# Kernel tuning notes

Measured on AMD Instinct MI355X. Metric: run time of the kernel, lower is better.

## Reference

```python
import jax, jax.numpy as jnp
import numpy as np

C = 256
NH = 8
G = 32  # groupnorm groups (min(32, C))
EPS = 1e-6


def setup_inputs() -> dict:
    key = jax.random.key(0)
    ks = jax.random.split(key, 7)
    B, D, H, W = 2, 16, 16, 16
    x = jax.random.normal(ks[0], (B, C, D, H, W), dtype=jnp.float32)
    gn_gamma = jnp.ones((C,), jnp.float32)
    gn_beta = jnp.zeros((C,), jnp.float32)
    s = 1.0 / np.sqrt(C)
    qkv_w = jax.random.normal(ks[1], (3 * C, C), jnp.float32) * s  # 1x1x1 conv weight
    qkv_b = jnp.zeros((3 * C,), jnp.float32)
    proj_w = jax.random.normal(ks[2], (C, C), jnp.float32) * s
    proj_b = jnp.zeros((C,), jnp.float32)
    return {"x": x, "gn_gamma": gn_gamma, "gn_beta": gn_beta,
            "qkv_w": qkv_w, "qkv_b": qkv_b, "proj_w": proj_w, "proj_b": proj_b}


def _group_norm(x, gamma, beta):
    # x: [B, C, S]
    B, Cc, S = x.shape
    xg = x.reshape(B, G, (Cc // G) * S)
    mu = xg.mean(axis=-1, keepdims=True)
    var = xg.var(axis=-1, keepdims=True)
    xg = (xg - mu) * jax.lax.rsqrt(var + EPS)
    x = xg.reshape(B, Cc, S)
    return x * gamma[None, :, None] + beta[None, :, None]


def reference(x, gn_gamma, gn_beta, qkv_w, qkv_b, proj_w, proj_b):
    B, Cc, D, H, W = x.shape
    S = D * H * W
    hd = Cc // NH
    xf = x.reshape(B, Cc, S)
    h = _group_norm(xf, gn_gamma, gn_beta)
    # 1x1x1 conv == channel matmul: [B, 3C, S]
    qkv = jnp.einsum('oc,bcs->bos', qkv_w, h) + qkv_b[None, :, None]
    # torch path: reshape(B,3C,S).permute(0,2,1).chunk -> q=channels[0:C]
    q, k, v = qkv[:, :Cc], qkv[:, Cc:2 * Cc], qkv[:, 2 * Cc:]
    # [B, C, S] -> [B, NH, S, hd]
    def to_heads(t):
        return t.reshape(B, NH, hd, S).transpose(0, 1, 3, 2)
    q, k, v = to_heads(q), to_heads(k), to_heads(v)
    scale = hd ** (-0.5)
    attn = jax.nn.softmax(jnp.einsum('bnqd,bnkd->bnqk', q, k) * scale, axis=-1)
    o = jnp.einsum('bnqk,bnkd->bnqd', attn, v)  # [B, NH, S, hd]
    o = o.transpose(0, 1, 3, 2).reshape(B, Cc, S)  # back to [B, C, S]
    o = jnp.einsum('oc,bcs->bos', proj_w, o) + proj_b[None, :, None]
    return x + o.reshape(B, Cc, D, H, W)
```

## Files before the change

### kernel.cpp

```cpp
#include <hip/hip_runtime.h>
#include <cstddef>

#define S_LEN 4096
#define C_DIM 256
#define NHEADS 8
#define HDIM 32

typedef __attribute__((ext_vector_type(8))) _Float16 half8;
typedef __attribute__((ext_vector_type(4))) _Float16 half4;
typedef __attribute__((ext_vector_type(2))) _Float16 h2t;
typedef __attribute__((ext_vector_type(2))) __fp16 fp16x2;
typedef __attribute__((ext_vector_type(4))) float floatx4;

#define SC2F ((float)(0.17677669529663687 * 1.4426950408889634))

__global__ __launch_bounds__(256) void prep_stats(
    const float* __restrict__ qkv_w, const float* __restrict__ proj_w,
    const float* __restrict__ qkv_b, const float* __restrict__ x,
    _Float16* __restrict__ wq, _Float16* __restrict__ wp,
    float* __restrict__ qbias, float* __restrict__ pstat)
{
  const int blk = blockIdx.x;
  const int tid = threadIdx.x;
  if (blk < 512) {
    __shared__ float red[2][4];
    const int gb = blk >> 3, e = blk & 7;
    const int g = gb & 31, b = gb >> 5;
    const float* xb = x + ((size_t)b * C_DIM + g * 8) * S_LEN + e * 4096;
    const float4* x4 = (const float4*)xb;
    float sum = 0.f, sumsq = 0.f;
    #pragma unroll
    for (int i = 0; i < 4; ++i) {
      float4 v = x4[tid + i * 256];
      sum += v.x + v.y + v.z + v.w;
      sumsq += v.x * v.x + v.y * v.y + v.z * v.z + v.w * v.w;
    }
    for (int off = 1; off < 64; off <<= 1) {
      sum += __shfl_xor(sum, off, 64);
      sumsq += __shfl_xor(sumsq, off, 64);
    }
    const int wv = tid >> 6, lane = tid & 63;
    if (lane == 0) { red[0][wv] = sum; red[1][wv] = sumsq; }
    __syncthreads();
    if (tid == 0) {
      pstat[(gb * 8 + e) * 2 + 0] = red[0][0] + red[0][1] + red[0][2] + red[0][3];
      pstat[(gb * 8 + e) * 2 + 1] = red[1][0] + red[1][1] + red[1][2] + red[1][3];
    }
  } else if (blk < 704) {
    const int i = (blk - 512) * 1024 + tid * 4;
    float4 v = *(const float4*)(qkv_w + i);
    const float sc = (i < 65536) ? SC2F : 1.f;
    half4 h = { (_Float16)(v.x * sc), (_Float16)(v.y * sc),
                (_Float16)(v.z * sc), (_Float16)(v.w * sc) };
    *(half4*)(wq + i) = h;
  } else if (blk < 768) {
    const int i = (blk - 704) * 1024 + tid * 4;
    float4 v = *(const float4*)(proj_w + i);
    half4 h = { (_Float16)v.x, (_Float16)v.y, (_Float16)v.z, (_Float16)v.w };
    *(half4*)(wp + i) = h;
  } else {
    #pragma unroll
    for (int j = 0; j < 3; ++j) {
      const int i = tid + j * 256;
      float bv = qkv_b[i];
      if (i < 256) bv *= SC2F;
      qbias[i] = bv;
    }
  }
}

__global__ __launch_bounds__(512) void qkv_gn_gemm(
    const _Float16* __restrict__ W, const float* __restrict__ bias,
    const float* __restrict__ x, const float* __restrict__ gamma,
    const float* __restrict__ beta, const float* __restrict__ pstat,
    _Float16* __restrict__ qo, _Float16* __restrict__ ko_,
    _Float16* __restrict__ vo)
{
  __shared__ __align__(16) _Float16 Ld[256 * 40];
  const int tid = threadIdx.x;
  const int b = blockIdx.y;
  const int s0 = blockIdx.x * 32;

  {
    const int c0 = (tid & 127) * 2, c1 = c0 + 1;
    const int sh = tid >> 7;
    const int gb = b * 32 + (c0 >> 3);
    float s = 0.f, sq = 0.f;
    #pragma unroll
    for (int e = 0; e < 8; ++e) {
      s  += pstat[(gb * 8 + e) * 2 + 0];
      sq += pstat[(gb * 8 + e) * 2 + 1];
    }
    const float mean = s * (1.f / 32768.f);
    const float rstd = rsqrtf(sq * (1.f / 32768.f) - mean * mean + 1e-6f);
    const float ga0 = gamma[c0] * rstd, be0 = beta[c0] - mean * ga0;
    const float ga1 = gamma[c1] * rstd, be1 = beta[c1] - mean * ga1;
    const float4* xa = (const float4*)(x + ((size_t)b * C_DIM + c0) * S_LEN + s0 + sh * 8);
    const float4* xc = (const float4*)(x + ((size_t)b * C_DIM + c1) * S_LEN + s0 + sh * 8);
    #pragma unroll
    for (int j = 0; j < 2; ++j) {
      float4 a = xa[j], c = xc[j];
      int sl = sh * 8 + j * 4;
      *(h2t*)&Ld[(sl + 0) * 264 + c0] = (h2t){ (_Float16)(a.x * ga0 + be0), (_Float16)(c.x * ga1 + be1) };
      *(h2t*)&Ld[(sl + 1) * 264 + c0] = (h2t){ (_Float16)(a.y * ga0 + be0), (_Float16)(c.y * ga1 + be1) };
      *(h2t*)&Ld[(sl + 2) * 264 + c0] = (h2t){ (_Float16)(a.z * ga0 + be0), (_Float16)(c.z * ga1 + be1) };
      *(h2t*)&Ld[(sl + 3) * 264 + c0] = (h2t){ (_Float16)(a.w * ga0 + be0), (_Float16)(c.w * ga1 + be1) };
    }
  }
  __syncthreads();

  const int lane = tid & 63, wv = tid >> 6;
  const int m = lane & 15, quad = lane >> 4;
  const _Float16* wrow[6];
  #pragma unroll
  for (int j = 0; j < 6; ++j)
    wrow[j] = W + (size_t)((wv + 8 * j) * 16 + m) * C_DIM + quad * 8;
  const _Float16* lp = &Ld[m * 264 + quad * 8];

  floatx4 acc[6][2];
  #pragma unroll
  for (int j = 0; j < 6; ++j) {
    acc[j][0] = (floatx4){0.f,0.f,0.f,0.f};
    acc[j][1] = (floatx4){0.f,0.f,0.f,0.f};
  }

  #pragma unroll 2
  for (int k0 = 0; k0 < C_DIM; k0 += 32) {
    half8 b0 = *(const half8*)(lp + k0);
    half8 b1 = *(const half8*)(lp + 16 * 264 + k0);
    #pragma unroll
    for (int j = 0; j < 6; ++j) {
      half8 a = *(const half8*)(wrow[j] + k0);
      acc[j][0] = __builtin_amdgcn_mfma_f32_16x16x32_f16(a, b0, acc[j][0], 0, 0, 0);
      acc[j][1] = __builtin_amdgcn_mfma_f32_16x16x32_f16(a, b1, acc[j][1], 0, 0, 0);
    }
  }

  __syncthreads();
  #pragma unroll
  for (int j = 0; j < 4; ++j) {
    const int ob = (wv + 8 * j) * 16 + quad * 4;
    const float bv0 = bias[ob], bv1 = bias[ob + 1],
                bv2 = bias[ob + 2], bv3 = bias[ob + 3];
    _Float16* dst = (ob < 256) ? qo : ko_;
    const int oo = ob & 255, n = oo >> 5, d0 = oo & 31;
    #pragma unroll
    for (int sub = 0; sub < 2; ++sub) {
      int s = s0 + sub * 16 + m;
      half4 h = { (_Float16)(acc[j][sub][0] + bv0), (_Float16)(acc[j][sub][1] + bv1),
                  (_Float16)(acc[j][sub][2] + bv2), (_Float16)(acc[j][sub][3] + bv3) };
      *(half4*)(dst + (((size_t)b * NHEADS + n) * S_LEN + s) * HDIM + d0) = h;
    }
  }
  _Float16* VLd = Ld;
  #pragma unroll
  for (int j = 4; j < 6; ++j) {
    const int ob = (wv + 8 * j) * 16 + quad * 4;
    const int lch = ob - 512;
    const float bv0 = bias[ob], bv1 = bias[ob + 1],
                bv2 = bias[ob + 2], bv3 = bias[ob + 3];
    #pragma unroll
    for (int sub = 0; sub < 2; ++sub) {
      int s = sub * 16 + m;
      VLd[(lch + 0) * 40 + s] = (_Float16)(acc[j][sub][0] + bv0);
      VLd[(lch + 1) * 40 + s] = (_Float16)(acc[j][sub][1] + bv1);
      VLd[(lch + 2) * 40 + s] = (_Float16)(acc[j][sub][2] + bv2);
      VLd[(lch + 3) * 40 + s] = (_Float16)(acc[j][sub][3] + bv3);
    }
  }
  __syncthreads();
  {
    const int ch = tid >> 1, sh = tid & 1;
    const int n = ch >> 5, d = ch & 31;
    _Float16* dst = vo + ((size_t)(b * NHEADS + n) * HDIM + d) * S_LEN + s0 + sh * 16;
    const _Float16* src = VLd + ch * 40 + sh * 16;
    *(half8*)(dst + 0) = *(const half8*)(src + 0);
    *(half8*)(dst + 8) = *(const half8*)(src + 8);
  }
}

__global__ __launch_bounds__(512) void attn_kernel(
    const _Float16* __restrict__ q, const _Float16* __restrict__ k,
    const _Float16* __restrict__ v, _Float16* __restrict__ o)
{
  __shared__ __align__(16) _Float16 Kl[2][128 * 40];
  __shared__ __align__(16) _Float16 Vl[2][32 * 136];
  const int tid = threadIdx.x;
  const int lane = tid & 63, wv = tid >> 6;
  const int m = lane & 15, quad = lane >> 4;
  const int n = blockIdx.y, b = blockIdx.z;
  const int qc = blockIdx.x;
  const int q0 = qc * 256 + wv * 32;
  const int bh = b * NHEADS + n;

  const _Float16* qb = q + (size_t)bh * S_LEN * HDIM;
  const _Float16* kb = k + (size_t)bh * S_LEN * HDIM;
  const _Float16* vb = v + (size_t)bh * HDIM * S_LEN;

  half8 qfA = *(const half8*)(qb + (size_t)(q0 + m) * HDIM + quad * 8);
  half8 qfB = *(const half8*)(qb + (size_t)(q0 + 16 + m) * HDIM + quad * 8);

  const int krow = wv * 16 + (lane >> 2), kc = (lane & 3) * 8;
  const int vrow = wv * 4 + (lane >> 4), vc = (lane & 15) * 8;
  const _Float16* kg = kb + (size_t)krow * HDIM + kc;
  const _Float16* vg = vb + (size_t)vrow * S_LEN + vc;
  const int klds = krow * 40 + kc;
  const int vlds = vrow * 136 + vc;

  int4 kreg = *(const int4*)kg;
  int4 vreg = *(const int4*)vg;
  const _Float16* kgp = kg + 128 * HDIM;
  const _Float16* vgp = vg + 128;

  floatx4 oA0 = {0.f,0.f,0.f,0.f}, oA1 = oA0, oB0 = oA0, oB1 = oA0;
  float lA0 = 0.f, lA1 = 0.f, lB0 = 0.f, lB1 = 0.f;
  const fp16x2 one2 = { (__fp16)1.0f, (__fp16)1.0f };
  const floatx4 zz = {0.f,0.f,0.f,0.f};

  #pragma unroll 2
  for (int it = 0; it < 32; ++it) {
    const int bufi = it & 1;
    *(int4*)(&Kl[bufi][klds]) = kreg;
    *(int4*)(&Vl[bufi][vlds]) = vreg;
    kreg = *(const int4*)kgp; kgp += 128 * HDIM;
    vreg = *(const int4*)vgp; vgp += 128;
    __syncthreads();
    const _Float16* Kb = Kl[bufi];
    const _Float16* Vb = Vl[bufi];

    #pragma unroll
    for (int t = 0; t < 8; ++t) {
      const int tt = (t + wv) & 7;
      half8 kf  = *(const half8*)(Kb + (tt * 16 + m) * 40 + quad * 8);
      half4 vf0 = *(const half4*)(Vb + m * 136 + tt * 16 + quad * 4);
      half4 vf1 = *(const half4*)(Vb + (16 + m) * 136 + tt * 16 + quad * 4);
      __builtin_amdgcn_s_setprio(1);
      floatx4 sA = __builtin_amdgcn_mfma_f32_16x16x32_f16(kf, qfA, zz, 0, 0, 0);
      floatx4 sB = __builtin_amdgcn_mfma_f32_16x16x32_f16(kf, qfB, zz, 0, 0, 0);
      __builtin_amdgcn_s_setprio(0);
      float eA0 = __builtin_amdgcn_exp2f(sA[0]);
      float eA1 = __builtin_amdgcn_exp2f(sA[1]);
      float eA2 = __builtin_amdgcn_exp2f(sA[2]);
      float eA3 = __builtin_amdgcn_exp2f(sA[3]);
      float eB0 = __builtin_amdgcn_exp2f(sB[0]);
      float eB1 = __builtin_amdgcn_exp2f(sB[1]);
      float eB2 = __builtin_amdgcn_exp2f(sB[2]);
      float eB3 = __builtin_amdgcn_exp2f(sB[3]);
      half4 pA, pB;
      fp16x2 pAlo = __builtin_amdgcn_cvt_pkrtz(eA0, eA1);
      fp16x2 pAhi = __builtin_amdgcn_cvt_pkrtz(eA2, eA3);
      fp16x2 pBlo = __builtin_amdgcn_cvt_pkrtz(eB0, eB1);
      fp16x2 pBhi = __builtin_amdgcn_cvt_pkrtz(eB2, eB3);
      *(fp16x2*)&pA = pAlo; *((fp16x2*)&pA + 1) = pAhi;
      *(fp16x2*)&pB = pBlo; *((fp16x2*)&pB + 1) = pBhi;
      lA0 = __builtin_amdgcn_fdot2(pAlo, one2, lA0, false);
      lA1 = __builtin_amdgcn_fdot2(pAhi, one2, lA1, false);
      lB0 = __builtin_amdgcn_fdot2(pBlo, one2, lB0, false);
      lB1 = __builtin_amdgcn_fdot2(pBhi, one2, lB1, false);
      __builtin_amdgcn_s_setprio(1);
      oA0 = __builtin_amdgcn_mfma_f32_16x16x16f16(vf0, pA, oA0, 0, 0, 0);
      oA1 = __builtin_amdgcn_mfma_f32_16x16x16f16(vf1, pA, oA1, 0, 0, 0);
      oB0 = __builtin_amdgcn_mfma_f32_16x16x16f16(vf0, pB, oB0, 0, 0, 0);
      oB1 = __builtin_amdgcn_mfma_f32_16x16x16f16(vf1, pB, oB1, 0, 0, 0);
      __builtin_amdgcn_s_setprio(0);
    }
  }
  float lA = lA0 + lA1, lB = lB0 + lB1;
  lA += __shfl_xor(lA, 16, 64); lA += __shfl_xor(lA, 32, 64);
  lB += __shfl_xor(lB, 16, 64); lB += __shfl_xor(lB, 32, 64);
  const float rA = 1.f / lA, rB = 1.f / lB;
  _Float16* obase = o + ((size_t)bh * S_LEN) * HDIM;
  {
    _Float16* oh = obase + (size_t)(q0 + m) * HDIM;
    half4 h0 = { (_Float16)(oA0[0] * rA), (_Float16)(oA0[1] * rA),
                 (_Float16)(oA0[2] * rA), (_Float16)(oA0[3] * rA) };
    half4 h1 = { (_Float16)(oA1[0] * rA), (_Float16)(oA1[1] * rA),
                 (_Float16)(oA1[2] * rA), (_Float16)(oA1[3] * rA) };
    *(half4*)(oh + quad * 4) = h0;
    *(half4*)(oh + 16 + quad * 4) = h1;
  }
  {
    _Float16* oh = obase + (size_t)(q0 + 16 + m) * HDIM;
    half4 h0 = { (_Float16)(oB0[0] * rB), (_Float16)(oB0[1] * rB),
                 (_Float16)(oB0[2] * rB), (_Float16)(oB0[3] * rB) };
    half4 h1 = { (_Float16)(oB1[0] * rB), (_Float16)(oB1[1] * rB),
                 (_Float16)(oB1[2] * rB), (_Float16)(oB1[3] * rB) };
    *(half4*)(oh + quad * 4) = h0;
    *(half4*)(oh + 16 + quad * 4) = h1;
  }
}

__global__ __launch_bounds__(256) void proj_gemm(
    const _Float16* __restrict__ W, const float* __restrict__ bias,
    const _Float16* __restrict__ o,
    const float* __restrict__ x, float* __restrict__ out)
{
  const int tid = threadIdx.x;
  const int lane = tid & 63, wv = tid >> 6;
  const int m = lane & 15, quad = lane >> 4;
  const int mtb = blockIdx.x * 8 + wv * 2;
  const int s0 = blockIdx.y * 64;
  const int b = blockIdx.z;

  const _Float16* wrow0 = W + (size_t)((mtb + 0) * 16 + m) * C_DIM + quad * 8;
  const _Float16* wrow1 = W + (size_t)((mtb + 1) * 16 + m) * C_DIM + quad * 8;
  floatx4 acc[2][4];
  #pragma unroll
  for (int j = 0; j < 2; ++j)
    #pragma unroll
    for (int s = 0; s < 4; ++s) acc[j][s] = (floatx4){0.f,0.f,0.f,0.f};

  #pragma unroll
  for (int k0 = 0; k0 < C_DIM; k0 += 32) {
    const int n = k0 >> 5;
    const int d0 = quad * 8;
    half8 bf[4];
    #pragma unroll
    for (int sub = 0; sub < 4; ++sub) {
      size_t idx = (((size_t)(b * NHEADS + n)) * S_LEN + s0 + sub * 16 + m) * HDIM + d0;
      bf[sub] = *(const half8*)(o + idx);
    }
    half8 af0 = *(const half8*)(wrow0 + k0);
    half8 af1 = *(const half8*)(wrow1 + k0);
    #pragma unroll
    for (int sub = 0; sub < 4; ++sub) {
      acc[0][sub] = __builtin_amdgcn_mfma_f32_16x16x32_f16(af0, bf[sub], acc[0][sub], 0, 0, 0);
      acc[1][sub] = __builtin_amdgcn_mfma_f32_16x16x32_f16(af1, bf[sub], acc[1][sub], 0, 0, 0);
    }
  }
  #pragma unroll
  for (int j = 0; j < 2; ++j)
    #pragma unroll
    for (int sub = 0; sub < 4; ++sub) {
      int s = s0 + sub * 16 + m;
      #pragma unroll
      for (int r = 0; r < 4; ++r) {
        int c = (mtb + j) * 16 + quad * 4 + r;
        size_t idx = ((size_t)b * C_DIM + c) * S_LEN + s;
        out[idx] = x[idx] + acc[j][sub][r] + bias[c];
      }
    }
}

extern "C" void kernel_launch(void* const* d_in, const int* in_sizes, int n_in,
                              void* d_out, int out_size, void* d_ws, size_t ws_size,
                              hipStream_t stream) {
  const float* x        = (const float*)d_in[0];
  const float* gn_gamma = (const float*)d_in[1];
  const float* gn_beta  = (const float*)d_in[2];
  const float* qkv_w    = (const float*)d_in[3];
  const float* qkv_b    = (const float*)d_in[4];
  const float* proj_w   = (const float*)d_in[5];
  const float* proj_b   = (const float*)d_in[6];
  float* out = (float*)d_out;

  const size_t n1 = (size_t)2 * S_LEN * C_DIM;
  char* ws = (char*)d_ws;
  _Float16* qx  = (_Float16*)ws;
  _Float16* kx  = qx + n1;
  _Float16* vx  = kx + n1;
  _Float16* wq  = vx + n1;
  _Float16* wp  = wq + 768 * 256;
  float*    qbias = (float*)(wp + 256 * 256);
  float*    pstat = qbias + 768;
  _Float16* ox  = (_Float16*)(pstat + 1024);

  prep_stats<<<769, 256, 0, stream>>>(qkv_w, proj_w, qkv_b, x, wq, wp, qbias, pstat);
  qkv_gn_gemm<<<dim3(128, 2), 512, 0, stream>>>(wq, qbias, x, gn_gamma, gn_beta, pstat, qx, kx, vx);
  attn_kernel<<<dim3(16, 8, 2), 512, 0, stream>>>(qx, kx, vx, ox);
  proj_gemm<<<dim3(2, 64, 2), 256, 0, stream>>>(wp, proj_b, ox, x, out);
}
```

Measured before the change: 144.6 us.

## Fuse all four stages into one cooperative persistent kernel with grid syncs

Merges the prep/stats, QKV GEMM with groupnorm, attention and projection kernels into one cooperative kernel of 256 blocks. Grid-wide syncs separate the stages, so the four separate launches and the gaps between them go away. The work is remapped per stage: stats jobs run two per block and the projection uses smaller tiles. In exchange, grid syncs and a fixed 256-block grid limit parallelism in stages that previously used more blocks, and one shared-memory allocation is reused across all stages.

```diff
diff --git a/kernel.cpp b/kernel.cpp
--- a/kernel.cpp
+++ b/kernel.cpp
@@ -1,5 +1,8 @@
 #include <hip/hip_runtime.h>
+#include <hip/hip_cooperative_groups.h>
 #include <cstddef>
+
+namespace cg = cooperative_groups;
 
 #define S_LEN 4096
 #define C_DIM 256
@@ -14,24 +17,54 @@
 
 #define SC2F ((float)(0.17677669529663687 * 1.4426950408889634))
 
-__global__ __launch_bounds__(256) void prep_stats(
-    const float* __restrict__ qkv_w, const float* __restrict__ proj_w,
-    const float* __restrict__ qkv_b, const float* __restrict__ x,
+__global__ __launch_bounds__(512) void fused_all(
+    const float* __restrict__ x, const float* __restrict__ gamma,
+    const float* __restrict__ beta, const float* __restrict__ qkv_w,
+    const float* __restrict__ qkv_b, const float* __restrict__ proj_w,
+    const float* __restrict__ proj_b, float* __restrict__ out,
     _Float16* __restrict__ wq, _Float16* __restrict__ wp,
-    float* __restrict__ qbias, float* __restrict__ pstat)
+    float* __restrict__ qbias, float* __restrict__ pstat,
+    _Float16* __restrict__ qx, _Float16* __restrict__ kx,
+    _Float16* __restrict__ vx, _Float16* __restrict__ ox)
 {
-  const int blk = blockIdx.x;
+  cg::grid_group grid = cg::this_grid();
+  __shared__ __align__(16) char smem[37888];
   const int tid = threadIdx.x;
-  if (blk < 512) {
-    __shared__ float red[2][4];
-    const int gb = blk >> 3, e = blk & 7;
+  const int bid = blockIdx.x;
+  const int lane = tid & 63, wv = tid >> 6;
+  const int m = lane & 15, quad = lane >> 4;
+
+  {
+    const int gi = bid * 512 + tid;
+    const int i = gi * 2;
+    if (i < 196608) {
+      float2 v = *(const float2*)(qkv_w + i);
+      const float sc = (i < 65536) ? SC2F : 1.f;
+      *(h2t*)(wq + i) = (h2t){ (_Float16)(v.x * sc), (_Float16)(v.y * sc) };
+    } else {
+      const int j = i - 196608;
+      float2 v = *(const float2*)(proj_w + j);
+      *(h2t*)(wp + j) = (h2t){ (_Float16)v.x, (_Float16)v.y };
+    }
+    if (bid == 0 && tid < 256) {
+      #pragma unroll
+      for (int j = 0; j < 3; ++j) {
+        const int i2 = tid + j * 256;
+        float bv = qkv_b[i2];
+        if (i2 < 256) bv *= SC2F;
+        qbias[i2] = bv;
+      }
+    }
+    float* red = (float*)smem;
+    const int h = tid >> 8, t = tid & 255;
+    const int job = bid * 2 + h;
+    const int gb = job >> 3, e = job & 7;
     const int g = gb & 31, b = gb >> 5;
-    const float* xb = x + ((size_t)b * C_DIM + g * 8) * S_LEN + e * 4096;
-    const float4* x4 = (const float4*)xb;
+    const float4* x4 = (const float4*)(x + ((size_t)b * C_DIM + g * 8) * S_LEN + e * 4096);
     float sum = 0.f, sumsq = 0.f;
     #pragma unroll
-    for (int i = 0; i < 4; ++i) {
-      float4 v = x4[tid + i * 256];
+    for (int i2 = 0; i2 < 4; ++i2) {
+      float4 v = x4[t + i2 * 256];
       sum += v.x + v.y + v.z + v.w;
       sumsq += v.x * v.x + v.y * v.y + v.z * v.z + v.w * v.w;
     }
@@ -39,307 +72,264 @@
       sum += __shfl_xor(sum, off, 64);
       sumsq += __shfl_xor(sumsq, off, 64);
     }
-    const int wv = tid >> 6, lane = tid & 63;
-    if (lane == 0) { red[0][wv] = sum; red[1][wv] = sumsq; }
+    const int w4 = (tid >> 6) & 3;
+    if (lane == 0) { red[(h * 2 + 0) * 4 + w4] = sum; red[(h * 2 + 1) * 4 + w4] = sumsq; }
     __syncthreads();
-    if (tid == 0) {
-      pstat[(gb * 8 + e) * 2 + 0] = red[0][0] + red[0][1] + red[0][2] + red[0][3];
-      pstat[(gb * 8 + e) * 2 + 1] = red[1][0] + red[1][1] + red[1][2] + red[1][3];
-    }
-  } else if (blk < 704) {
-    const int i = (blk - 512) * 1024 + tid * 4;
-    float4 v = *(const float4*)(qkv_w + i);
-    const float sc = (i < 65536) ? SC2F : 1.f;
-    half4 h = { (_Float16)(v.x * sc), (_Float16)(v.y * sc),
-                (_Float16)(v.z * sc), (_Float16)(v.w * sc) };
-    *(half4*)(wq + i) = h;
-  } else if (blk < 768) {
-    const int i = (blk - 704) * 1024 + tid * 4;
-    float4 v = *(const float4*)(proj_w + i);
-    half4 h = { (_Float16)v.x, (_Float16)v.y, (_Float16)v.z, (_Float16)v.w };
-    *(half4*)(wp + i) = h;
-  } else {
-    #pragma unroll
-    for (int j = 0; j < 3; ++j) {
-      const int i = tid + j * 256;
-      float bv = qkv_b[i];
-      if (i < 256) bv *= SC2F;
-      qbias[i] = bv;
+    if (t == 0) {
+      pstat[job * 2 + 0] = red[(h*2+0)*4+0] + red[(h*2+0)*4+1] + red[(h*2+0)*4+2] + red[(h*2+0)*4+3];
+      pstat[job * 2 + 1] = red[(h*2+1)*4+0] + red[(h*2+1)*4+1] + red[(h*2+1)*4+2] + red[(h*2+1)*4+3];
     }
   }
-}
-
-__global__ __launch_bounds__(512) void qkv_gn_gemm(
-    const _Float16* __restrict__ W, const float* __restrict__ bias,
-    const float* __restrict__ x, const float* __restrict__ gamma,
-    const float* __restrict__ beta, const float* __restrict__ pstat,
-    _Float16* __restrict__ qo, _Float16* __restrict__ ko_,
-    _Float16* __restrict__ vo)
-{
-  __shared__ __align__(16) _Float16 Ld[256 * 40];
-  const int tid = threadIdx.x;
-  const int b = blockIdx.y;
-  const int s0 = blockIdx.x * 32;
+  __threadfence();
+  grid.sync();
 
   {
-    const int c0 = (tid & 127) * 2, c1 = c0 + 1;
-    const int sh = tid >> 7;
-    const int gb = b * 32 + (c0 >> 3);
-    float s = 0.f, sq = 0.f;
-    #pragma unroll
-    for (int e = 0; e < 8; ++e) {
-      s  += pstat[(gb * 8 + e) * 2 + 0];
-      sq += pstat[(gb * 8 + e) * 2 + 1];
-    }
-    const float mean = s * (1.f / 32768.f);
-    const float rstd = rsqrtf(sq * (1.f / 32768.f) - mean * mean + 1e-6f);
-    const float ga0 = gamma[c0] * rstd, be0 = beta[c0] - mean * ga0;
-    const float ga1 = gamma[c1] * rstd, be1 = beta[c1] - mean * ga1;
-    const float4* xa = (const float4*)(x + ((size_t)b * C_DIM + c0) * S_LEN + s0 + sh * 8);
-    const float4* xc = (const float4*)(x + ((size_t)b * C_DIM + c1) * S_LEN + s0 + sh * 8);
-    #pragma unroll
-    for (int j = 0; j < 2; ++j) {
-      float4 a = xa[j], c = xc[j];
-      int sl = sh * 8 + j * 4;
-      *(h2t*)&Ld[(sl + 0) * 264 + c0] = (h2t){ (_Float16)(a.x * ga0 + be0), (_Float16)(c.x * ga1 + be1) };
-      *(h2t*)&Ld[(sl + 1) * 264 + c0] = (h2t){ (_Float16)(a.y * ga0 + be0), (_Float16)(c.y * ga1 + be1) };
-      *(h2t*)&Ld[(sl + 2) * 264 + c0] = (h2t){ (_Float16)(a.z * ga0 + be0), (_Float16)(c.z * ga1 + be1) };
-      *(h2t*)&Ld[(sl + 3) * 264 + c0] = (h2t){ (_Float16)(a.w * ga0 + be0), (_Float16)(c.w * ga1 + be1) };
+    _Float16* Ld = (_Float16*)smem;
+    const int b = bid >> 7;
+    const int s0 = (bid & 127) * 32;
+    {
+      const int c0 = (tid & 127) * 2, c1 = c0 + 1;
+      const int sh = tid >> 7;
+      const int gb = b * 32 + (c0 >> 3);
+      float s = 0.f, sq = 0.f;
+      #pragma unroll
+      for (int e = 0; e < 8; ++e) {
+        s  += pstat[(gb * 8 + e) * 2 + 0];
+        sq += pstat[(gb * 8 + e) * 2 + 1];
+      }
+      const float mean = s * (1.f / 32768.f);
+      const float rstd = rsqrtf(sq * (1.f / 32768.f) - mean * mean + 1e-6f);
+      const float ga0 = gamma[c0] * rstd, be0 = beta[c0] - mean * ga0;
+      const float ga1 = gamma[c1] * rstd, be1 = beta[c1] - mean * ga1;
+      const float4* xa = (const float4*)(x + ((size_t)b * C_DIM + c0) * S_LEN + s0 + sh * 8);
+      const float4* xc = (const float4*)(x + ((size_t)b * C_DIM + c1) * S_LEN + s0 + sh * 8);
+      #pragma unroll
+      for (int j = 0; j < 2; ++j) {
+        float4 a = xa[j], c = xc[j];
+        int sl = sh * 8 + j * 4;
+        *(h2t*)&Ld[(sl + 0) * 264 + c0] = (h2t){ (_Float16)(a.x * ga0 + be0), (_Float16)(c.x * ga1 + be1) };
+        *(h2t*)&Ld[(sl + 1) * 264 + c0] = (h2t){ (_Float16)(a.y * ga0 + be0), (_Float16)(c.y * ga1 + be1) };
+        *(h2t*)&Ld[(sl + 2) * 264 + c0] = (h2t){ (_Float16)(a.z * ga0 + be0), (_Float16)(c.z * ga1 + be1) };
+        *(h2t*)&Ld[(sl + 3) * 264 + c0] = (h2t){ (_Float16)(a.w * ga0 + be0), (_Float16)(c.w * ga1 + be1) };
+      }
+    }
+    __syncthreads();
+
+    const _Float16* wrow[6];
+    #pragma unroll
+    for (int j = 0; j < 6; ++j)
+      wrow[j] = wq + (size_t)((wv + 8 * j) * 16 + m) * C_DIM + quad * 8;
+    const _Float16* lp = &Ld[m * 264 + quad * 8];
+
+    floatx4 acc[6][2];
+    #pragma unroll
+    for (int j = 0; j < 6; ++j) {
+      acc[j][0] = (floatx4){0.f,0.f,0.f,0.f};
+      acc[j][1] = (floatx4){0.f,0.f,0.f,0.f};
+    }
+    #pragma unroll 2
+    for (int k0 = 0; k0 < C_DIM; k0 += 32) {
+      half8 b0 = *(const half8*)(lp + k0);
+      half8 b1 = *(const half8*)(lp + 16 * 264 + k0);
+      #pragma unroll
+      for (int j = 0; j < 6; ++j) {
+        half8 a = *(const half8*)(wrow[j] + k0);
+        acc[j][0] = __builtin_amdgcn_mfma_f32_16x16x32_f16(a, b0, acc[j][0], 0, 0, 0);
+        acc[j][1] = __builtin_amdgcn_mfma_f32_16x16x32_f16(a, b1, acc[j][1], 0, 0, 0);
+      }
+    }
+    __syncthreads();
+    #pragma unroll
+    for (int j = 0; j < 4; ++j) {
+      const int ob = (wv + 8 * j) * 16 + quad * 4;
+      const float bv0 = qbias[ob], bv1 = qbias[ob + 1],
+                  bv2 = qbias[ob + 2], bv3 = qbias[ob + 3];
+      _Float16* dst = (ob < 256) ? qx : kx;
+      const int oo = ob & 255, n = oo >> 5, d0 = oo & 31;
+      #pragma unroll
+      for (int sub = 0; sub < 2; ++sub) {
+        int s = s0 + sub * 16 + m;
+        half4 h = { (_Float16)(acc[j][sub][0] + bv0), (_Float16)(acc[j][sub][1] + bv1),
+                    (_Float16)(acc[j][sub][2] + bv2), (_Float16)(acc[j][sub][3] + bv3) };
+        *(half4*)(dst + (((size_t)b * NHEADS + n) * S_LEN + s) * HDIM + d0) = h;
+      }
+    }
+    _Float16* VLd = Ld;
+    #pragma unroll
+    for (int j = 4; j < 6; ++j) {
+      const int ob = (wv + 8 * j) * 16 + quad * 4;
+      const int lch = ob - 512;
+      const float bv0 = qbias[ob], bv1 = qbias[ob + 1],
+                  bv2 = qbias[ob + 2], bv3 = qbias[ob + 3];
+      #pragma unroll
+      for (int sub = 0; sub < 2; ++sub) {
+        int s = sub * 16 + m;
+        VLd[(lch + 0) * 40 + s] = (_Float16)(acc[j][sub][0] + bv0);
+        VLd[(lch + 1) * 40 + s] = (_Float16)(acc[j][sub][1] + bv1);
+        VLd[(lch + 2) * 40 + s] = (_Float16)(acc[j][sub][2] + bv2);
+        VLd[(lch + 3) * 40 + s] = (_Float16)(acc[j][sub][3] + bv3);
+      }
+    }
+    __syncthreads();
+    {
+      const int ch = tid >> 1, sh = tid & 1;
+      const int n = ch >> 5, d = ch & 31;
+      _Float16* dst = vx + ((size_t)(b * NHEADS + n) * HDIM + d) * S_LEN + s0 + sh * 16;
+      const _Float16* src = VLd + ch * 40 + sh * 16;
+      *(half8*)(dst + 0) = *(const half8*)(src + 0);
+      *(half8*)(dst + 8) = *(const half8*)(src + 8);
     }
   }
-  __syncthreads();
-
-  const int lane = tid & 63, wv = tid >> 6;
-  const int m = lane & 15, quad = lane >> 4;
-  const _Float16* wrow[6];
-  #pragma unroll
-  for (int j = 0; j < 6; ++j)
-    wrow[j] = W + (size_t)((wv + 8 * j) * 16 + m) * C_DIM + quad * 8;
-  const _Float16* lp = &Ld[m * 264 + quad * 8];
-
-  floatx4 acc[6][2];
-  #pragma unroll
-  for (int j = 0; j < 6; ++j) {
-    acc[j][0] = (floatx4){0.f,0.f,0.f,0.f};
-    acc[j][1] = (floatx4){0.f,0.f,0.f,0.f};
+  __threadfence();
+  grid.sync();
+
+  {
+    _Float16* KlB = (_Float16*)smem;
+    _Float16* VlB = (_Float16*)(smem + 20480);
+    const int qc = bid & 15, n = (bid >> 4) & 7, b = bid >> 7;
+    const int q0 = qc * 256 + wv * 32;
+    const int bh = b * NHEADS + n;
+
+    const _Float16* qb = qx + (size_t)bh * S_LEN * HDIM;
+    const _Float16* kb = kx + (size_t)bh * S_LEN * HDIM;
+    const _Float16* vb = vx + (size_t)bh * HDIM * S_LEN;
+
+    half8 qfA = *(const half8*)(qb + (size_t)(q0 + m) * HDIM + quad * 8);
+    half8 qfB = *(const half8*)(qb + (size_t)(q0 + 16 + m) * HDIM + quad * 8);
+
+    const int krow = wv * 16 + (lane >> 2), kc = (lane & 3) * 8;
+    const int vrow = wv * 4 + (lane >> 4), vc = (lane & 15) * 8;
+    const _Float16* kg = kb + (size_t)krow * HDIM + kc;
+    const _Float16* vg = vb + (size_t)vrow * S_LEN + vc;
+    const int klds = krow * 40 + kc;
+    const int vlds = vrow * 136 + vc;
+
+    int4 kreg = *(const int4*)kg;
+    int4 vreg = *(const int4*)vg;
+    const _Float16* kgp = kg + 128 * HDIM;
+    const _Float16* vgp = vg + 128;
+
+    floatx4 oA0 = {0.f,0.f,0.f,0.f}, oA1 = oA0, oB0 = oA0, oB1 = oA0;
+    float lA0 = 0.f, lA1 = 0.f, lB0 = 0.f, lB1 = 0.f;
+    const fp16x2 one2 = { (__fp16)1.0f, (__fp16)1.0f };
+    const floatx4 zz = {0.f,0.f,0.f,0.f};
+
+    #pragma unroll 2
+    for (int it = 0; it < 32; ++it) {
+      const int bufi = it & 1;
+      *(int4*)(KlB + bufi * 5120 + klds) = kreg;
+      *(int4*)(VlB + bufi * 4352 + vlds) = vreg;
+      kreg = *(const int4*)kgp; kgp += 128 * HDIM;
+      vreg = *(const int4*)vgp; vgp += 128;
+      __syncthreads();
+      const _Float16* Kb = KlB + bufi * 5120;
+      const _Float16* Vb = VlB + bufi * 4352;
+
+      #pragma unroll
+      for (int t = 0; t < 8; ++t) {
+        const int tt = (t + wv) & 7;
+        half8 kf  = *(const half8*)(Kb + (tt * 16 + m) * 40 + quad * 8);
+        half4 vf0 = *(const half4*)(Vb + m * 136 + tt * 16 + quad * 4);
+        half4 vf1 = *(const half4*)(Vb + (16 + m) * 136 + tt * 16 + quad * 4);
+        __builtin_amdgcn_s_setprio(1);
+        floatx4 sA = __builtin_amdgcn_mfma_f32_16x16x32_f16(kf, qfA, zz, 0, 0, 0);
+        floatx4 sB = __builtin_amdgcn_mfma_f32_16x16x32_f16(kf, qfB, zz, 0, 0, 0);
+        __builtin_amdgcn_s_setprio(0);
+        float eA0 = __builtin_amdgcn_exp2f(sA[0]);
+        float eA1 = __builtin_amdgcn_exp2f(sA[1]);
+        float eA2 = __builtin_amdgcn_exp2f(sA[2]);
+        float eA3 = __builtin_amdgcn_exp2f(sA[3]);
+        float eB0 = __builtin_amdgcn_exp2f(sB[0]);
+        float eB1 = __builtin_amdgcn_exp2f(sB[1]);
+        float eB2 = __builtin_amdgcn_exp2f(sB[2]);
+        float eB3 = __builtin_amdgcn_exp2f(sB[3]);
+        half4 pA, pB;
+        fp16x2 pAlo = __builtin_amdgcn_cvt_pkrtz(eA0, eA1);
+        fp16x2 pAhi = __builtin_amdgcn_cvt_pkrtz(eA2, eA3);
+        fp16x2 pBlo = __builtin_amdgcn_cvt_pkrtz(eB0, eB1);
+        fp16x2 pBhi = __builtin_amdgcn_cvt_pkrtz(eB2, eB3);
+        *(fp16x2*)&pA = pAlo; *((fp16x2*)&pA + 1) = pAhi;
+        *(fp16x2*)&pB = pBlo; *((fp16x2*)&pB + 1) = pBhi;
+        lA0 = __builtin_amdgcn_fdot2(pAlo, one2, lA0, false);
+        lA1 = __builtin_amdgcn_fdot2(pAhi, one2, lA1, false);
+        lB0 = __builtin_amdgcn_fdot2(pBlo, one2, lB0, false);
+        lB1 = __builtin_amdgcn_fdot2(pBhi, one2, lB1, false);
+        __builtin_amdgcn_s_setprio(1);
+        oA0 = __builtin_amdgcn_mfma_f32_16x16x16f16(vf0, pA, oA0, 0, 0, 0);
+        oA1 = __builtin_amdgcn_mfma_f32_16x16x16f16(vf1, pA, oA1, 0, 0, 0);
+        oB0 = __builtin_amdgcn_mfma_f32_16x16x16f16(vf0, pB, oB0, 0, 0, 0);
+        oB1 = __builtin_amdgcn_mfma_f32_16x16x16f16(vf1, pB, oB1, 0, 0, 0);
+        __builtin_amdgcn_s_setprio(0);
+      }
+    }
+    float lA = lA0 + lA1, lB = lB0 + lB1;
+    lA += __shfl_xor(lA, 16, 64); lA += __shfl_xor(lA, 32, 64);
+    lB += __shfl_xor(lB, 16, 64); lB += __shfl_xor(lB, 32, 64);
+    const float rA = 1.f / lA, rB = 1.f / lB;
+    _Float16* obase = ox + ((size_t)bh * S_LEN) * HDIM;
+    {
+      _Float16* oh = obase + (size_t)(q0 + m) * HDIM;
+      half4 h0 = { (_Float16)(oA0[0] * rA), (_Float16)(oA0[1] * rA),
+                   (_Float16)(oA0[2] * rA), (_Float16)(oA0[3] * rA) };
+      half4 h1 = { (_Float16)(oA1[0] * rA), (_Float16)(oA1[1] * rA),
+                   (_Float16)(oA1[2] * rA), (_Float16)(oA1[3] * rA) };
+      *(half4*)(oh + quad * 4) = h0;
+      *(half4*)(oh + 16 + quad * 4) = h1;
+    }
+    {
+      _Float16* oh = obase + (size_t)(q0 + 16 + m) * HDIM;
+      half4 h0 = { (_Float16)(oB0[0] * rB), (_Float16)(oB0[1] * rB),
+                   (_Float16)(oB0[2] * rB), (_Float16)(oB0[3] * rB) };
+      half4 h1 = { (_Float16)(oB1[0] * rB), (_Float16)(oB1[1] * rB),
+                   (_Float16)(oB1[2] * rB), (_Float16)(oB1[3] * rB) };
+      *(half4*)(oh + quad * 4) = h0;
+      *(half4*)(oh + 16 + quad * 4) = h1;
+    }
   }
-
-  #pragma unroll 2
-  for (int k0 = 0; k0 < C_DIM; k0 += 32) {
-    half8 b0 = *(const half8*)(lp + k0);
-    half8 b1 = *(const half8*)(lp + 16 * 264 + k0);
-    #pragma unroll
-    for (int j = 0; j < 6; ++j) {
-      half8 a = *(const half8*)(wrow[j] + k0);
-      acc[j][0] = __builtin_amdgcn_mfma_f32_16x16x32_f16(a, b0, acc[j][0], 0, 0, 0);
-      acc[j][1] = __builtin_amdgcn_mfma_f32_16x16x32_f16(a, b1, acc[j][1], 0, 0, 0);
-    }
+  __threadfence();
+  grid.sync();
+
+  {
+    const int b = bid >> 7;
+    const int s0 = (bid & 127) * 32;
+    const int mtb = wv * 2;
+    const _Float16* wrow0 = wp + (size_t)((mtb + 0) * 16 + m) * C_DIM + quad * 8;
+    const _Float16* wrow1 = wp + (size_t)((mtb + 1) * 16 + m) * C_DIM + quad * 8;
+    floatx4 acc[2][2];
+    acc[0][0] = (floatx4){0.f,0.f,0.f,0.f}; acc[0][1] = acc[0][0];
+    acc[1][0] = acc[0][0]; acc[1][1] = acc[0][0];
+
+    #pragma unroll
+    for (int k0 = 0; k0 < C_DIM; k0 += 32) {
+      const int n = k0 >> 5;
+      const int d0 = quad * 8;
+      half8 bf[2];
+      #pragma unroll
+      for (int sub = 0; sub < 2; ++sub) {
+        size_t idx = (((size_t)(b * NHEADS + n)) * S_LEN + s0 + sub * 16 + m) * HDIM + d0;
+        bf[sub] = *(const half8*)(ox + idx);
+      }
+      half8 af0 = *(const half8*)(wrow0 + k0);
+      half8 af1 = *(const half8*)(wrow1 + k0);
+      #pragma unroll
+      for (int sub = 0; sub < 2; ++sub) {
+        acc[0][sub] = __builtin_amdgcn_mfma_f32_16x16x32_f16(af0, bf[sub], acc[0][sub], 0, 0, 0);
+        acc[1][sub] = __builtin_amdgcn_mfma_f32_16x16x32_f16(af1, bf[sub], acc[1][sub], 0, 0, 0);
+      }
+    }
+    #pragma unroll
+    for (int j = 0; j < 2; ++j)
+      #pragma unroll
+      for (int sub = 0; sub < 2; ++sub) {
+        int s = s0 + sub * 16 + m;
+        #pragma unroll
+        for (int r = 0; r < 4; ++r) {
+          int c = (mtb + j) * 16 + quad * 4 + r;
+          size_t idx = ((size_t)b * C_DIM + c) * S_LEN + s;
+          out[idx] = x[idx] + acc[j][sub][r] + proj_b[c];
+        }
+      }
   }
-
-  __syncthreads();
-  #pragma unroll
-  for (int j = 0; j < 4; ++j) {
-    const int ob = (wv + 8 * j) * 16 + quad * 4;
-    const float bv0 = bias[ob], bv1 = bias[ob + 1],
-                bv2 = bias[ob + 2], bv3 = bias[ob + 3];
-    _Float16* dst = (ob < 256) ? qo : ko_;
-    const int oo = ob & 255, n = oo >> 5, d0 = oo & 31;
-    #pragma unroll
-    for (int sub = 0; sub < 2; ++sub) {
-      int s = s0 + sub * 16 + m;
-      half4 h = { (_Float16)(acc[j][sub][0] + bv0), (_Float16)(acc[j][sub][1] + bv1),
-                  (_Float16)(acc[j][sub][2] + bv2), (_Float16)(acc[j][sub][3] + bv3) };
-      *(half4*)(dst + (((size_t)b * NHEADS + n) * S_LEN + s) * HDIM + d0) = h;
-    }
-  }
-  _Float16* VLd = Ld;
-  #pragma unroll
-  for (int j = 4; j < 6; ++j) {
-    const int ob = (wv + 8 * j) * 16 + quad * 4;
-    const int lch = ob - 512;
-    const float bv0 = bias[ob], bv1 = bias[ob + 1],
-                bv2 = bias[ob + 2], bv3 = bias[ob + 3];
-    #pragma unroll
-    for (int sub = 0; sub < 2; ++sub) {
-      int s = sub * 16 + m;
-      VLd[(lch + 0) * 40 + s] = (_Float16)(acc[j][sub][0] + bv0);
-      VLd[(lch + 1) * 40 + s] = (_Float16)(acc[j][sub][1] + bv1);
-      VLd[(lch + 2) * 40 + s] = (_Float16)(acc[j][sub][2] + bv2);
-      VLd[(lch + 3) * 40 + s] = (_Float16)(acc[j][sub][3] + bv3);
-    }
-  }
-  __syncthreads();
-  {
-    const int ch = tid >> 1, sh = tid & 1;
-    const int n = ch >> 5, d = ch & 31;
-    _Float16* dst = vo + ((size_t)(b * NHEADS + n) * HDIM + d) * S_LEN + s0 + sh * 16;
-    const _Float16* src = VLd + ch * 40 + sh * 16;
-    *(half8*)(dst + 0) = *(const half8*)(src + 0);
-    *(half8*)(dst + 8) = *(const half8*)(src + 8);
-  }
-}
-
-__global__ __launch_bounds__(512) void attn_kernel(
-    const _Float16* __restrict__ q, const _Float16* __restrict__ k,
-    const _Float16* __restrict__ v, _Float16* __restrict__ o)
-{
-  __shared__ __align__(16) _Float16 Kl[2][128 * 40];
-  __shared__ __align__(16) _Float16 Vl[2][32 * 136];
-  const int tid = threadIdx.x;
-  const int lane = tid & 63, wv = tid >> 6;
-  const int m = lane & 15, quad = lane >> 4;
-  const int n = blockIdx.y, b = blockIdx.z;
-  const int qc = blockIdx.x;
-  const int q0 = qc * 256 + wv * 32;
-  const int bh = b * NHEADS + n;
-
-  const _Float16* qb = q + (size_t)bh * S_LEN * HDIM;
-  const _Float16* kb = k + (size_t)bh * S_LEN * HDIM;
-  const _Float16* vb = v + (size_t)bh * HDIM * S_LEN;
-
-  half8 qfA = *(const half8*)(qb + (size_t)(q0 + m) * HDIM + quad * 8);
-  half8 qfB = *(const half8*)(qb + (size_t)(q0 + 16 + m) * HDIM + quad * 8);
-
-  const int krow = wv * 16 + (lane >> 2), kc = (lane & 3) * 8;
-  const int vrow = wv * 4 + (lane >> 4), vc = (lane & 15) * 8;
-  const _Float16* kg = kb + (size_t)krow * HDIM + kc;
-  const _Float16* vg = vb + (size_t)vrow * S_LEN + vc;
-  const int klds = krow * 40 + kc;
-  const int vlds = vrow * 136 + vc;
-
-  int4 kreg = *(const int4*)kg;
-  int4 vreg = *(const int4*)vg;
-  const _Float16* kgp = kg + 128 * HDIM;
-  const _Float16* vgp = vg + 128;
-
-  floatx4 oA0 = {0.f,0.f,0.f,0.f}, oA1 = oA0, oB0 = oA0, oB1 = oA0;
-  float lA0 = 0.f, lA1 = 0.f, lB0 = 0.f, lB1 = 0.f;
-  const fp16x2 one2 = { (__fp16)1.0f, (__fp16)1.0f };
-  const floatx4 zz = {0.f,0.f,0.f,0.f};
-
-  #pragma unroll 2
-  for (int it = 0; it < 32; ++it) {
-    const int bufi = it & 1;
-    *(int4*)(&Kl[bufi][klds]) = kreg;
-    *(int4*)(&Vl[bufi][vlds]) = vreg;
-    kreg = *(const int4*)kgp; kgp += 128 * HDIM;
-    vreg = *(const int4*)vgp; vgp += 128;
-    __syncthreads();
-    const _Float16* Kb = Kl[bufi];
-    const _Float16* Vb = Vl[bufi];
-
-    #pragma unroll
-    for (int t = 0; t < 8; ++t) {
-      const int tt = (t + wv) & 7;
-      half8 kf  = *(const half8*)(Kb + (tt * 16 + m) * 40 + quad * 8);
-      half4 vf0 = *(const half4*)(Vb + m * 136 + tt * 16 + quad * 4);
-      half4 vf1 = *(const half4*)(Vb + (16 + m) * 136 + tt * 16 + quad * 4);
-      __builtin_amdgcn_s_setprio(1);
-      floatx4 sA = __builtin_amdgcn_mfma_f32_16x16x32_f16(kf, qfA, zz, 0, 0, 0);
-      floatx4 sB = __builtin_amdgcn_mfma_f32_16x16x32_f16(kf, qfB, zz, 0, 0, 0);
-      __builtin_amdgcn_s_setprio(0);
-      float eA0 = __builtin_amdgcn_exp2f(sA[0]);
-      float eA1 = __builtin_amdgcn_exp2f(sA[1]);
-      float eA2 = __builtin_amdgcn_exp2f(sA[2]);
-      float eA3 = __builtin_amdgcn_exp2f(sA[3]);
-      float eB0 = __builtin_amdgcn_exp2f(sB[0]);
-      float eB1 = __builtin_amdgcn_exp2f(sB[1]);
-      float eB2 = __builtin_amdgcn_exp2f(sB[2]);
-      float eB3 = __builtin_amdgcn_exp2f(sB[3]);
-      half4 pA, pB;
-      fp16x2 pAlo = __builtin_amdgcn_cvt_pkrtz(eA0, eA1);
-      fp16x2 pAhi = __builtin_amdgcn_cvt_pkrtz(eA2, eA3);
-      fp16x2 pBlo = __builtin_amdgcn_cvt_pkrtz(eB0, eB1);
-      fp16x2 pBhi = __builtin_amdgcn_cvt_pkrtz(eB2, eB3);
-      *(fp16x2*)&pA = pAlo; *((fp16x2*)&pA + 1) = pAhi;
-      *(fp16x2*)&pB = pBlo; *((fp16x2*)&pB + 1) = pBhi;
-      lA0 = __builtin_amdgcn_fdot2(pAlo, one2, lA0, false);
-      lA1 = __builtin_amdgcn_fdot2(pAhi, one2, lA1, false);
-      lB0 = __builtin_amdgcn_fdot2(pBlo, one2, lB0, false);
-      lB1 = __builtin_amdgcn_fdot2(pBhi, one2, lB1, false);
-      __builtin_amdgcn_s_setprio(1);
-      oA0 = __builtin_amdgcn_mfma_f32_16x16x16f16(vf0, pA, oA0, 0, 0, 0);
-      oA1 = __builtin_amdgcn_mfma_f32_16x16x16f16(vf1, pA, oA1, 0, 0, 0);
-      oB0 = __builtin_amdgcn_mfma_f32_16x16x16f16(vf0, pB, oB0, 0, 0, 0);
-      oB1 = __builtin_amdgcn_mfma_f32_16x16x16f16(vf1, pB, oB1, 0, 0, 0);
-      __builtin_amdgcn_s_setprio(0);
-    }
-  }
-  float lA = lA0 + lA1, lB = lB0 + lB1;
-  lA += __shfl_xor(lA, 16, 64); lA += __shfl_xor(lA, 32, 64);
-  lB += __shfl_xor(lB, 16, 64); lB += __shfl_xor(lB, 32, 64);
-  const float rA = 1.f / lA, rB = 1.f / lB;
-  _Float16* obase = o + ((size_t)bh * S_LEN) * HDIM;
-  {
-    _Float16* oh = obase + (size_t)(q0 + m) * HDIM;
-    half4 h0 = { (_Float16)(oA0[0] * rA), (_Float16)(oA0[1] * rA),
-                 (_Float16)(oA0[2] * rA), (_Float16)(oA0[3] * rA) };
-    half4 h1 = { (_Float16)(oA1[0] * rA), (_Float16)(oA1[1] * rA),
-                 (_Float16)(oA1[2] * rA), (_Float16)(oA1[3] * rA) };
-    *(half4*)(oh + quad * 4) = h0;
-    *(half4*)(oh + 16 + quad * 4) = h1;
-  }
-  {
-    _Float16* oh = obase + (size_t)(q0 + 16 + m) * HDIM;
-    half4 h0 = { (_Float16)(oB0[0] * rB), (_Float16)(oB0[1] * rB),
-                 (_Float16)(oB0[2] * rB), (_Float16)(oB0[3] * rB) };
-    half4 h1 = { (_Float16)(oB1[0] * rB), (_Float16)(oB1[1] * rB),
-                 (_Float16)(oB1[2] * rB), (_Float16)(oB1[3] * rB) };
-    *(half4*)(oh + quad * 4) = h0;
-    *(half4*)(oh + 16 + quad * 4) = h1;
-  }
-}
-
-__global__ __launch_bounds__(256) void proj_gemm(
-    const _Float16* __restrict__ W, const float* __restrict__ bias,
-    const _Float16* __restrict__ o,
-    const float* __restrict__ x, float* __restrict__ out)
-{
-  const int tid = threadIdx.x;
-  const int lane = tid & 63, wv = tid >> 6;
-  const int m = lane & 15, quad = lane >> 4;
-  const int mtb = blockIdx.x * 8 + wv * 2;
-  const int s0 = blockIdx.y * 64;
-  const int b = blockIdx.z;
-
-  const _Float16* wrow0 = W + (size_t)((mtb + 0) * 16 + m) * C_DIM + quad * 8;
-  const _Float16* wrow1 = W + (size_t)((mtb + 1) * 16 + m) * C_DIM + quad * 8;
-  floatx4 acc[2][4];
-  #pragma unroll
-  for (int j = 0; j < 2; ++j)
-    #pragma unroll
-    for (int s = 0; s < 4; ++s) acc[j][s] = (floatx4){0.f,0.f,0.f,0.f};
-
-  #pragma unroll
-  for (int k0 = 0; k0 < C_DIM; k0 += 32) {
-    const int n = k0 >> 5;
-    const int d0 = quad * 8;
-    half8 bf[4];
-    #pragma unroll
-    for (int sub = 0; sub < 4; ++sub) {
-      size_t idx = (((size_t)(b * NHEADS + n)) * S_LEN + s0 + sub * 16 + m) * HDIM + d0;
-      bf[sub] = *(const half8*)(o + idx);
-    }
-    half8 af0 = *(const half8*)(wrow0 + k0);
-    half8 af1 = *(const half8*)(wrow1 + k0);
-    #pragma unroll
-    for (int sub = 0; sub < 4; ++sub) {
-      acc[0][sub] = __builtin_amdgcn_mfma_f32_16x16x32_f16(af0, bf[sub], acc[0][sub], 0, 0, 0);
-      acc[1][sub] = __builtin_amdgcn_mfma_f32_16x16x32_f16(af1, bf[sub], acc[1][sub], 0, 0, 0);
-    }
-  }
-  #pragma unroll
-  for (int j = 0; j < 2; ++j)
-    #pragma unroll
-    for (int sub = 0; sub < 4; ++sub) {
-      int s = s0 + sub * 16 + m;
-      #pragma unroll
-      for (int r = 0; r < 4; ++r) {
-        int c = (mtb + j) * 16 + quad * 4 + r;
-        size_t idx = ((size_t)b * C_DIM + c) * S_LEN + s;
-        out[idx] = x[idx] + acc[j][sub][r] + bias[c];
-      }
-    }
 }
 
 extern "C" void kernel_launch(void* const* d_in, const int* in_sizes, int n_in,
@@ -365,8 +355,12 @@
   float*    pstat = qbias + 768;
   _Float16* ox  = (_Float16*)(pstat + 1024);
 
-  prep_stats<<<769, 256, 0, stream>>>(qkv_w, proj_w, qkv_b, x, wq, wp, qbias, pstat);
-  qkv_gn_gemm<<<dim3(128, 2), 512, 0, stream>>>(wq, qbias, x, gn_gamma, gn_beta, pstat, qx, kx, vx);
-  attn_kernel<<<dim3(16, 8, 2), 512, 0, stream>>>(qx, kx, vx, ox);
-  proj_gemm<<<dim3(2, 64, 2), 256, 0, stream>>>(wp, proj_b, ox, x, out);
+  void* args[] = {
+    (void*)&x, (void*)&gn_gamma, (void*)&gn_beta, (void*)&qkv_w,
+    (void*)&qkv_b, (void*)&proj_w, (void*)&proj_b, (void*)&out,
+    (void*)&wq, (void*)&wp, (void*)&qbias, (void*)&pstat,
+    (void*)&qx, (void*)&kx, (void*)&vx, (void*)&ox
+  };
+  hipLaunchCooperativeKernel((const void*)fused_all, dim3(256), dim3(512),
+                             args, 0, stream);
 }
```

After: 380.9 us. 163% more time.
